# Optimization experiments

Measured on AMD Instinct MI355X. Metric: run time of the kernel, lower is better.

## Reference

```python
import jax, jax.numpy as jnp
import numpy as np

N, E = 100000, 1600000
D_IN, H, C = 128, 4, 32
NEG_SLOPE = 0.2

def setup_inputs() -> dict:
    key = jax.random.key(0)
    ks = jax.random.split(key, 6)
    x = jax.random.normal(ks[0], (N, D_IN), dtype=jnp.float32)
    edge_index = jax.random.randint(ks[1], (2, E), 0, N, dtype=jnp.int64)
    s = 1.0 / np.sqrt(D_IN)
    W_l = jax.random.normal(ks[2], (D_IN, H * C), dtype=jnp.float32) * s
    W_r = jax.random.normal(ks[3], (D_IN, H * C), dtype=jnp.float32) * s
    att = jax.random.normal(ks[4], (H, C), dtype=jnp.float32) * (1.0 / np.sqrt(C))
    bias = jax.random.normal(ks[5], (H * C,), dtype=jnp.float32) * 0.01
    return {"x": x, "edge_index": edge_index, "W_l": W_l, "W_r": W_r, "att": att, "bias": bias}

def reference(x, edge_index, W_l, W_r, att, bias):
    # GATv2: e_ij = att . LeakyReLU(W_l x_j + W_r x_i); softmax over incoming edges of i;
    # out_i = sum_j alpha_ij * (W_l x_j); heads concatenated, then bias.
    src, dst = edge_index[0], edge_index[1]
    n = x.shape[0]
    xl = (x @ W_l).reshape(n, H, C)   # source transform (lin_l)
    xr = (x @ W_r).reshape(n, H, C)   # target transform (lin_r)
    xj = xl[src]                       # [E,H,C] gathered source feats
    xi = xr[dst]                       # [E,H,C] gathered target feats
    e = jax.nn.leaky_relu(xi + xj, NEG_SLOPE)
    score = jnp.einsum('ehc,hc->eh', e, att)          # [E,H]
    # segment softmax over destination nodes
    m = jax.ops.segment_max(score, dst, num_segments=n)  # [N,H]
    ex = jnp.exp(score - m[dst])
    denom = jax.ops.segment_sum(ex, dst, num_segments=n)  # [N,H]
    alpha = ex / (denom[dst] + 1e-16)                      # [E,H]
    out = jax.ops.segment_sum(alpha[..., None] * xj, dst, num_segments=n)  # [N,H,C]
    return out.reshape(n, H * C) + bias
```

## Files before the change

### kernel.cpp

```cpp
#include <hip/hip_runtime.h>
#include <hip/hip_bf16.h>
#include <math.h>

#define N_NODES 100000
#define E_EDGES 1600000
#define D 128
#define NEG_SLOPE 0.2f

#define BSH   8
#define NBKT  391
#define BCAP  4992
#define SC_EPB 8192
#define SC_EPT 32
#define SC_BLOCKS ((E_EDGES + SC_EPB - 1) / SC_EPB)

typedef __bf16 bf16x8 __attribute__((ext_vector_type(8)));
typedef float f32x4 __attribute__((ext_vector_type(4)));
typedef float f32x2 __attribute__((ext_vector_type(2)));

__device__ __forceinline__ float bf2f(unsigned short u) {
    union { unsigned int i; float f; } x; x.i = ((unsigned int)u) << 16; return x.f;
}
__device__ __forceinline__ unsigned short f2bf(float f) {
    union { float f; unsigned int i; } x; x.f = f;
    unsigned int r = x.i + 0x7fffu + ((x.i >> 16) & 1u);
    return (unsigned short)(r >> 16);
}
__device__ __forceinline__ void unpack4p(uint2 u, f32x2* lo, f32x2* hi) {
    union { unsigned int i; float f; } a, b, c, d;
    a.i = u.x << 16; b.i = u.x & 0xffff0000u;
    c.i = u.y << 16; d.i = u.y & 0xffff0000u;
    *lo = (f32x2){a.f, b.f}; *hi = (f32x2){c.f, d.f};
}
__device__ __forceinline__ f32x2 pabs(f32x2 v) {
    union { f32x2 f; unsigned int u[2]; } x; x.f = v;
    x.u[0] &= 0x7fffffffu; x.u[1] &= 0x7fffffffu;
    return x.f;
}

__global__ void GATv2Conv_56908316672629_kernel(
    const unsigned int* ei_words, int* flags,
    const float* __restrict__ Wl, const float* __restrict__ Wr,
    unsigned short* __restrict__ wtg, int* __restrict__ bcur)
{
    __shared__ int cnt_edge;
    const int tid = threadIdx.x;
    const int bid = blockIdx.x;

    if (bid == 0) {
        for (int i = tid; i < NBKT; i += 256) bcur[i] = 0;
    }
    if (bid == 1) {
        if (tid == 0) cnt_edge = 0;
        __syncthreads();
        unsigned int w = ei_words[2 * tid + 1];
        if (w != 0u) atomicAdd(&cnt_edge, 1);
        __syncthreads();
        if (tid == 0) flags[0] = (cnt_edge == 0) ? 1 : 0;
    }

    const int gid = bid * 256 + tid;
    const int sel = gid >> 14;
    const int rem = gid & 16383;
    const int k = rem >> 7, n = rem & 127;
    const float* W = sel ? Wr : Wl;
    wtg[(size_t)sel * 16384 + n * 128 + k] = f2bf(W[k * 128 + n]);
}

__global__ __launch_bounds__(256) void gemm_f32_kernel(
    const float* __restrict__ X,
    const unsigned short* __restrict__ wtg,
    unsigned short* __restrict__ xl, unsigned short* __restrict__ xr,
    const unsigned int* __restrict__ ei, const int* __restrict__ flags,
    int* __restrict__ bcur, unsigned int* __restrict__ pairbuf)
{
    __shared__ union {
        struct {
            unsigned short Xs[128][136];
            unsigned short Cst[64][136];
        } g;
        struct { int h[NBKT]; int gbase[NBKT]; } sc;
    } sm;

    const int tid = threadIdx.x;

    if (blockIdx.x < SC_BLOCKS) {
        int* h = sm.sc.h;
        int* gbase = sm.sc.gbase;
        const int is64 = flags[0];
        const long long e0 = (long long)blockIdx.x * SC_EPB;

        unsigned int sv[SC_EPT], dv[SC_EPT];
#pragma unroll
        for (int j = 0; j < SC_EPT; ++j) {
            long long e = e0 + j * 256 + tid;
            unsigned int s = 0u, d = 0xffffffffu;
            if (e < E_EDGES) {
                if (is64) {
                    s = ((const uint2*)ei)[e].x;
                    d = ((const uint2*)ei)[E_EDGES + e].x;
                } else {
                    s = ei[e];
                    d = ei[E_EDGES + e];
                }
                if (s >= N_NODES || d >= N_NODES) d = 0xffffffffu;
            }
            sv[j] = s; dv[j] = d;
        }

        for (int i = tid; i < NBKT; i += 256) h[i] = 0;
        __syncthreads();

#pragma unroll
        for (int j = 0; j < SC_EPT; ++j)
            if (dv[j] != 0xffffffffu) atomicAdd(&h[dv[j] >> BSH], 1);
        __syncthreads();

        for (int i = tid; i < NBKT; i += 256) {
            int c = h[i];
            gbase[i] = c ? atomicAdd(&bcur[i], c) : 0;
            h[i] = 0;
        }
        __syncthreads();

#pragma unroll
        for (int j = 0; j < SC_EPT; ++j) {
            unsigned int d = dv[j];
            if (d != 0xffffffffu) {
                int b = (int)(d >> BSH);
                int r = gbase[b] + atomicAdd(&h[b], 1);
                if (r < BCAP)
                    pairbuf[(size_t)b * BCAP + r] = sv[j] | ((d & 255u) << 24);
            }
        }
        return;
    }

    const int rowbase = (blockIdx.x - SC_BLOCKS) * 128;

    for (int c = tid; c < 4096; c += 256) {
        int r = c >> 5, k4 = (c & 31) << 2;
        int grow = rowbase + r;
        float4 v = make_float4(0.f, 0.f, 0.f, 0.f);
        if (grow < N_NODES) v = ((const float4*)(X + (size_t)grow * D))[c & 31];
        union { unsigned short us[4]; uint2 u2; } pk;
        pk.us[0] = f2bf(v.x); pk.us[1] = f2bf(v.y);
        pk.us[2] = f2bf(v.z); pk.us[3] = f2bf(v.w);
        *((uint2*)&sm.g.Xs[r][k4]) = pk.u2;
    }
    __syncthreads();

    const int wave = tid >> 6, lane = tid & 63;
    const int mrow = lane & 15, quad = lane >> 4;
    const int srow = tid >> 2, sseg = tid & 3;

    for (int sel = 0; sel < 2; ++sel) {
        const bf16x8* wt = (const bf16x8*)(wtg + (size_t)sel * 16384);
        unsigned short* out = sel ? xr : xl;

        f32x4 accA[8], accB[8];
#pragma unroll
        for (int i = 0; i < 8; ++i) {
            accA[i] = (f32x4){0.f, 0.f, 0.f, 0.f};
            accB[i] = (f32x4){0.f, 0.f, 0.f, 0.f};
        }

#pragma unroll
        for (int kk = 0; kk < 4; ++kk) {
            const int k0 = kk * 32 + quad * 8;
            bf16x8 afA = *(const bf16x8*)&sm.g.Xs[wave * 16 + mrow][k0];
            bf16x8 afB = *(const bf16x8*)&sm.g.Xs[64 + wave * 16 + mrow][k0];
            const bf16x8* wk = wt + mrow * 16 + kk * 4 + quad;
#pragma unroll
            for (int n0 = 0; n0 < 8; ++n0) {
                bf16x8 bfrag = wk[n0 * 256];
                accA[n0] = __builtin_amdgcn_mfma_f32_16x16x32_bf16(afA, bfrag, accA[n0], 0, 0, 0);
                accB[n0] = __builtin_amdgcn_mfma_f32_16x16x32_bf16(afB, bfrag, accB[n0], 0, 0, 0);
            }
        }

        __syncthreads();
        const int crow = wave * 16 + quad * 4;
#pragma unroll
        for (int n0 = 0; n0 < 8; ++n0) {
            int col = n0 * 16 + mrow;
#pragma unroll
            for (int r = 0; r < 4; ++r)
                sm.g.Cst[crow + r][col] = f2bf(accA[n0][r]);
        }
        __syncthreads();
        {
            int grow = rowbase + srow;
            if (grow < N_NODES) {
                uint4* dst = (uint4*)(out + (size_t)grow * D);
#pragma unroll
                for (int j = 0; j < 4; ++j)
                    dst[sseg * 4 + j] = *(const uint4*)&sm.g.Cst[srow][sseg * 32 + j * 8];
            }
        }

        __syncthreads();
#pragma unroll
        for (int n0 = 0; n0 < 8; ++n0) {
            int col = n0 * 16 + mrow;
#pragma unroll
            for (int r = 0; r < 4; ++r)
                sm.g.Cst[crow + r][col] = f2bf(accB[n0][r]);
        }
        __syncthreads();
        {
            int grow = rowbase + 64 + srow;
            if (grow < N_NODES) {
                uint4* dst = (uint4*)(out + (size_t)grow * D);
#pragma unroll
                for (int j = 0; j < 4; ++j)
                    dst[sseg * 4 + j] = *(const uint4*)&sm.g.Cst[srow][sseg * 32 + j * 8];
            }
        }
        __syncthreads();
    }
}

__global__ __launch_bounds__(1024) void bucket_sort_kernel(
    const int* __restrict__ bcur, unsigned int* __restrict__ pairbuf,
    int* __restrict__ rowstart, int* __restrict__ rowend)
{
    __shared__ unsigned int stage[BCAP];
    __shared__ int cnt[256];
    __shared__ int wsum[4];

    const int b = blockIdx.x;
    const int tid = threadIdx.x;
    int n = bcur[b]; if (n > BCAP) n = BCAP;
    unsigned int* buf = pairbuf + (size_t)b * BCAP;

    for (int i = tid; i < n; i += 1024) stage[i] = buf[i];
    if (tid < 256) cnt[tid] = 0;
    __syncthreads();

    for (int i = tid; i < n; i += 1024) atomicAdd(&cnt[stage[i] >> 24], 1);
    __syncthreads();

    const int lane = tid & 63, wid = tid >> 6;
    int v = 0, inc = 0;
    if (tid < 256) {
        v = cnt[tid];
        inc = v;
#pragma unroll
        for (int off = 1; off < 64; off <<= 1) {
            int u = __shfl_up(inc, off);
            if (lane >= off) inc += u;
        }
        if (lane == 63) wsum[wid] = inc;
    }
    __syncthreads();
    if (tid < 256) {
        int add = 0;
#pragma unroll
        for (int w = 0; w < 3; ++w)
            if (w < wid) add += wsum[w];
        const int myend = inc + add;
        const int mystart = myend - v;
        const int node = b * 256 + tid;
        if (node < N_NODES) {
            rowstart[node] = b * BCAP + mystart;
            rowend[node]   = b * BCAP + myend;
        }
        cnt[tid] = mystart;
    }
    __syncthreads();

    for (int i = tid; i < n; i += 1024) {
        unsigned int p = stage[i];
        int pos = atomicAdd(&cnt[p >> 24], 1);
        buf[pos] = p & 0x00FFFFFFu;
    }
}

__global__ __launch_bounds__(256) void aggregate_kernel(
    const unsigned short* __restrict__ xl, const unsigned short* __restrict__ xr,
    const int* __restrict__ rowstart, const int* __restrict__ rowend,
    const int* __restrict__ ssrc,
    const float* __restrict__ att, const float* __restrict__ bias,
    float* __restrict__ out)
{
    const int t = threadIdx.x & 31;
    const int node = blockIdx.x * 8 + (threadIdx.x >> 5);
    if (node >= N_NODES) return;
    const int f0 = t * 4;

    f32x2 xr0, xr1;
    unpack4p(*(const uint2*)&xr[(size_t)node * D + f0], &xr0, &xr1);
    const float4 av = *(const float4*)&att[f0];
    f32x2 a60 = (f32x2){0.6f * av.x, 0.6f * av.y};
    f32x2 a61 = (f32x2){0.6f * av.z, 0.6f * av.w};
    f32x2 a40 = (f32x2){0.4f * av.x, 0.4f * av.y};
    f32x2 a41 = (f32x2){0.4f * av.z, 0.4f * av.w};

    const uint2* xlp = (const uint2*)xl + (f0 >> 2);

    const int p0 = rowstart[node];
    const int p1 = rowend[node];

    float l = 0.f;
    f32x2 acc0 = (f32x2){0.f, 0.f}, acc1 = (f32x2){0.f, 0.f};

#define ESCORE(u, xa0, xa1, pe)                                   \
    {                                                             \
        unpack4p(u, &xa0, &xa1);                                  \
        f32x2 v0 = xa0 + xr0, v1 = xa1 + xr1;                     \
        f32x2 pp = v0 * a60;                                      \
        pp += pabs(v0) * a40;                                     \
        pp += v1 * a61;                                           \
        pp += pabs(v1) * a41;                                     \
        pe = pp.x + pp.y;                                         \
    }

    int p = p0;
    for (; p + 4 <= p1; p += 4) {
        int s0 = ssrc[p], s1 = ssrc[p + 1], s2 = ssrc[p + 2], s3 = ssrc[p + 3];
        uint2 u0 = xlp[(size_t)s0 * 32];
        uint2 u1 = xlp[(size_t)s1 * 32];
        uint2 u2 = xlp[(size_t)s2 * 32];
        uint2 u3 = xlp[(size_t)s3 * 32];
        f32x2 xa0, xa1, xb0, xb1, xc0, xc1, xd0, xd1;
        float e0, e1, e2, e3;
        ESCORE(u0, xa0, xa1, e0);
        ESCORE(u1, xb0, xb1, e1);
        ESCORE(u2, xc0, xc1, e2);
        ESCORE(u3, xd0, xd1, e3);
#pragma unroll
        for (int off = 1; off < 8; off <<= 1) {
            e0 += __shfl_xor(e0, off);
            e1 += __shfl_xor(e1, off);
            e2 += __shfl_xor(e2, off);
            e3 += __shfl_xor(e3, off);
        }
        float w0 = __expf(e0), w1 = __expf(e1), w2 = __expf(e2), w3 = __expf(e3);
        l += (w0 + w1) + (w2 + w3);
        acc0 += w0 * xa0; acc1 += w0 * xa1;
        acc0 += w1 * xb0; acc1 += w1 * xb1;
        acc0 += w2 * xc0; acc1 += w2 * xc1;
        acc0 += w3 * xd0; acc1 += w3 * xd1;
    }
    for (; p < p1; ++p) {
        int s0 = ssrc[p];
        uint2 u0 = xlp[(size_t)s0 * 32];
        f32x2 xa0, xa1;
        float e0;
        ESCORE(u0, xa0, xa1, e0);
#pragma unroll
        for (int off = 1; off < 8; off <<= 1) e0 += __shfl_xor(e0, off);
        float w0 = __expf(e0);
        l += w0;
        acc0 += w0 * xa0; acc1 += w0 * xa1;
    }
#undef ESCORE

    const float inv = (l > 0.f) ? (1.f / l) : 0.f;
    const float4 bv = *(const float4*)&bias[f0];
    float4 o;
    o.x = fmaf(acc0.x, inv, bv.x);
    o.y = fmaf(acc0.y, inv, bv.y);
    o.z = fmaf(acc1.x, inv, bv.z);
    o.w = fmaf(acc1.y, inv, bv.w);
    *(float4*)&out[(size_t)node * D + f0] = o;
}

extern "C" void kernel_launch(void* const* d_in, const int* in_sizes, int n_in,
                              void* d_out, int out_size, void* d_ws, size_t ws_size,
                              hipStream_t stream)
{
    const float*        X    = (const float*)d_in[0];
    const unsigned int* ei   = (const unsigned int*)d_in[1];
    const float*        Wl   = (const float*)d_in[2];
    const float*        Wr   = (const float*)d_in[3];
    const float*        att  = (const float*)d_in[4];
    const float*        bias = (const float*)d_in[5];

    char* ws = (char*)d_ws;
    size_t off = 0;
    unsigned short* xl = (unsigned short*)(ws + off); off += (size_t)N_NODES * D * 2;
    unsigned short* xr = (unsigned short*)(ws + off); off += (size_t)N_NODES * D * 2;
    unsigned int* pairbuf = (unsigned int*)(ws + off); off += (size_t)NBKT * BCAP * 4;
    int* rowstart = (int*)(ws + off); off += (size_t)N_NODES * 4;
    int* rowend   = (int*)(ws + off); off += (size_t)N_NODES * 4;
    int* bcur     = (int*)(ws + off); off += (size_t)((NBKT + 255) & ~255) * 4;
    int* flags    = (int*)(ws + off); off += 256;
    unsigned short* wtg = (unsigned short*)(ws + off); off += 2 * 128 * 128 * 2;

    const int gb = (N_NODES + 127) / 128;

    GATv2Conv_56908316672629_kernel<<<128, 256, 0, stream>>>(ei, flags, Wl, Wr, wtg, bcur);

    gemm_f32_kernel<<<SC_BLOCKS + gb, 256, 0, stream>>>(
        X, wtg, xl, xr, ei, flags, bcur, pairbuf);

    bucket_sort_kernel<<<NBKT, 1024, 0, stream>>>(bcur, pairbuf, rowstart, rowend);

    aggregate_kernel<<<(N_NODES + 7) / 8, 256, 0, stream>>>(
        xl, xr, rowstart, rowend, (const int*)pairbuf, att, bias, (float*)d_out);
}
```

Before: 246.2 us.

## Fuse bucket sort and aggregation into one kernel using shared-memory CSR

Merges the per-bucket counting sort with the attention aggregation. Each 1024-thread block sorts its bucket's edges into shared memory and then aggregates its 256 destination nodes, 32 at a time over 8 passes. This removes one kernel launch, the global write and reload of the sorted source indices, and the rowstart/rowend arrays. In exchange, aggregation parallelism falls to 391 blocks with heavy shared-memory use (about 42KB), which limits occupancy and latency hiding for the gathers compared with the previous 12500 small blocks.

```diff
diff --git a/kernel.cpp b/kernel.cpp
--- a/kernel.cpp
+++ b/kernel.cpp
@@ -221,18 +221,22 @@
     }
 }
 
-__global__ __launch_bounds__(1024) void bucket_sort_kernel(
-    const int* __restrict__ bcur, unsigned int* __restrict__ pairbuf,
-    int* __restrict__ rowstart, int* __restrict__ rowend)
+__global__ __launch_bounds__(1024) void sort_agg_kernel(
+    const int* __restrict__ bcur, const unsigned int* __restrict__ pairbuf,
+    const unsigned short* __restrict__ xl, const unsigned short* __restrict__ xr,
+    const float* __restrict__ att, const float* __restrict__ bias,
+    float* __restrict__ out)
 {
     __shared__ unsigned int stage[BCAP];
+    __shared__ int sorted[BCAP];
+    __shared__ int rs[256], re[256];
     __shared__ int cnt[256];
     __shared__ int wsum[4];
 
     const int b = blockIdx.x;
     const int tid = threadIdx.x;
     int n = bcur[b]; if (n > BCAP) n = BCAP;
-    unsigned int* buf = pairbuf + (size_t)b * BCAP;
+    const unsigned int* buf = pairbuf + (size_t)b * BCAP;
 
     for (int i = tid; i < n; i += 1024) stage[i] = buf[i];
     if (tid < 256) cnt[tid] = 0;
@@ -261,11 +265,8 @@
             if (w < wid) add += wsum[w];
         const int myend = inc + add;
         const int mystart = myend - v;
-        const int node = b * 256 + tid;
-        if (node < N_NODES) {
-            rowstart[node] = b * BCAP + mystart;
-            rowend[node]   = b * BCAP + myend;
-        }
+        rs[tid] = mystart;
+        re[tid] = myend;
         cnt[tid] = mystart;
     }
     __syncthreads();
@@ -273,37 +274,20 @@
     for (int i = tid; i < n; i += 1024) {
         unsigned int p = stage[i];
         int pos = atomicAdd(&cnt[p >> 24], 1);
-        buf[pos] = p & 0x00FFFFFFu;
-    }
-}
-
-__global__ __launch_bounds__(256) void aggregate_kernel(
-    const unsigned short* __restrict__ xl, const unsigned short* __restrict__ xr,
-    const int* __restrict__ rowstart, const int* __restrict__ rowend,
-    const int* __restrict__ ssrc,
-    const float* __restrict__ att, const float* __restrict__ bias,
-    float* __restrict__ out)
-{
-    const int t = threadIdx.x & 31;
-    const int node = blockIdx.x * 8 + (threadIdx.x >> 5);
-    if (node >= N_NODES) return;
+        sorted[pos] = (int)(p & 0x00FFFFFFu);
+    }
+    __syncthreads();
+
+    const int t = tid & 31;
+    const int hw = tid >> 5;
     const int f0 = t * 4;
 
-    f32x2 xr0, xr1;
-    unpack4p(*(const uint2*)&xr[(size_t)node * D + f0], &xr0, &xr1);
     const float4 av = *(const float4*)&att[f0];
-    f32x2 a60 = (f32x2){0.6f * av.x, 0.6f * av.y};
-    f32x2 a61 = (f32x2){0.6f * av.z, 0.6f * av.w};
-    f32x2 a40 = (f32x2){0.4f * av.x, 0.4f * av.y};
-    f32x2 a41 = (f32x2){0.4f * av.z, 0.4f * av.w};
-
+    const f32x2 a60 = (f32x2){0.6f * av.x, 0.6f * av.y};
+    const f32x2 a61 = (f32x2){0.6f * av.z, 0.6f * av.w};
+    const f32x2 a40 = (f32x2){0.4f * av.x, 0.4f * av.y};
+    const f32x2 a41 = (f32x2){0.4f * av.z, 0.4f * av.w};
     const uint2* xlp = (const uint2*)xl + (f0 >> 2);
-
-    const int p0 = rowstart[node];
-    const int p1 = rowend[node];
-
-    float l = 0.f;
-    f32x2 acc0 = (f32x2){0.f, 0.f}, acc1 = (f32x2){0.f, 0.f};
 
 #define ESCORE(u, xa0, xa1, pe)                                   \
     {                                                             \
@@ -316,55 +300,70 @@
         pe = pp.x + pp.y;                                         \
     }
 
-    int p = p0;
-    for (; p + 4 <= p1; p += 4) {
-        int s0 = ssrc[p], s1 = ssrc[p + 1], s2 = ssrc[p + 2], s3 = ssrc[p + 3];
-        uint2 u0 = xlp[(size_t)s0 * 32];
-        uint2 u1 = xlp[(size_t)s1 * 32];
-        uint2 u2 = xlp[(size_t)s2 * 32];
-        uint2 u3 = xlp[(size_t)s3 * 32];
-        f32x2 xa0, xa1, xb0, xb1, xc0, xc1, xd0, xd1;
-        float e0, e1, e2, e3;
-        ESCORE(u0, xa0, xa1, e0);
-        ESCORE(u1, xb0, xb1, e1);
-        ESCORE(u2, xc0, xc1, e2);
-        ESCORE(u3, xd0, xd1, e3);
-#pragma unroll
-        for (int off = 1; off < 8; off <<= 1) {
-            e0 += __shfl_xor(e0, off);
-            e1 += __shfl_xor(e1, off);
-            e2 += __shfl_xor(e2, off);
-            e3 += __shfl_xor(e3, off);
-        }
-        float w0 = __expf(e0), w1 = __expf(e1), w2 = __expf(e2), w3 = __expf(e3);
-        l += (w0 + w1) + (w2 + w3);
-        acc0 += w0 * xa0; acc1 += w0 * xa1;
-        acc0 += w1 * xb0; acc1 += w1 * xb1;
-        acc0 += w2 * xc0; acc1 += w2 * xc1;
-        acc0 += w3 * xd0; acc1 += w3 * xd1;
-    }
-    for (; p < p1; ++p) {
-        int s0 = ssrc[p];
-        uint2 u0 = xlp[(size_t)s0 * 32];
-        f32x2 xa0, xa1;
-        float e0;
-        ESCORE(u0, xa0, xa1, e0);
-#pragma unroll
-        for (int off = 1; off < 8; off <<= 1) e0 += __shfl_xor(e0, off);
-        float w0 = __expf(e0);
-        l += w0;
-        acc0 += w0 * xa0; acc1 += w0 * xa1;
+    for (int pass = 0; pass < 8; ++pass) {
+        const int local = pass * 32 + hw;
+        const int node = b * 256 + local;
+        if (node >= N_NODES) continue;
+
+        f32x2 xr0, xr1;
+        unpack4p(*(const uint2*)&xr[(size_t)node * D + f0], &xr0, &xr1);
+
+        const int p0 = rs[local];
+        const int p1 = re[local];
+
+        float l = 0.f;
+        f32x2 acc0 = (f32x2){0.f, 0.f}, acc1 = (f32x2){0.f, 0.f};
+
+        int p = p0;
+        for (; p + 4 <= p1; p += 4) {
+            int s0 = sorted[p], s1 = sorted[p + 1], s2 = sorted[p + 2], s3 = sorted[p + 3];
+            uint2 u0 = xlp[(size_t)s0 * 32];
+            uint2 u1 = xlp[(size_t)s1 * 32];
+            uint2 u2 = xlp[(size_t)s2 * 32];
+            uint2 u3 = xlp[(size_t)s3 * 32];
+            f32x2 xa0, xa1, xb0, xb1, xc0, xc1, xd0, xd1;
+            float e0, e1, e2, e3;
+            ESCORE(u0, xa0, xa1, e0);
+            ESCORE(u1, xb0, xb1, e1);
+            ESCORE(u2, xc0, xc1, e2);
+            ESCORE(u3, xd0, xd1, e3);
+#pragma unroll
+            for (int off = 1; off < 8; off <<= 1) {
+                e0 += __shfl_xor(e0, off);
+                e1 += __shfl_xor(e1, off);
+                e2 += __shfl_xor(e2, off);
+                e3 += __shfl_xor(e3, off);
+            }
+            float w0 = __expf(e0), w1 = __expf(e1), w2 = __expf(e2), w3 = __expf(e3);
+            l += (w0 + w1) + (w2 + w3);
+            acc0 += w0 * xa0; acc1 += w0 * xa1;
+            acc0 += w1 * xb0; acc1 += w1 * xb1;
+            acc0 += w2 * xc0; acc1 += w2 * xc1;
+            acc0 += w3 * xd0; acc1 += w3 * xd1;
+        }
+        for (; p < p1; ++p) {
+            int s0 = sorted[p];
+            uint2 u0 = xlp[(size_t)s0 * 32];
+            f32x2 xa0, xa1;
+            float e0;
+            ESCORE(u0, xa0, xa1, e0);
+#pragma unroll
+            for (int off = 1; off < 8; off <<= 1) e0 += __shfl_xor(e0, off);
+            float w0 = __expf(e0);
+            l += w0;
+            acc0 += w0 * xa0; acc1 += w0 * xa1;
+        }
+
+        const float inv = (l > 0.f) ? (1.f / l) : 0.f;
+        const float4 bv = *(const float4*)&bias[f0];
+        float4 o;
+        o.x = fmaf(acc0.x, inv, bv.x);
+        o.y = fmaf(acc0.y, inv, bv.y);
+        o.z = fmaf(acc1.x, inv, bv.z);
+        o.w = fmaf(acc1.y, inv, bv.w);
+        *(float4*)&out[(size_t)node * D + f0] = o;
     }
 #undef ESCORE
-
-    const float inv = (l > 0.f) ? (1.f / l) : 0.f;
-    const float4 bv = *(const float4*)&bias[f0];
-    float4 o;
-    o.x = fmaf(acc0.x, inv, bv.x);
-    o.y = fmaf(acc0.y, inv, bv.y);
-    o.z = fmaf(acc1.x, inv, bv.z);
-    o.w = fmaf(acc1.y, inv, bv.w);
-    *(float4*)&out[(size_t)node * D + f0] = o;
 }
 
 extern "C" void kernel_launch(void* const* d_in, const int* in_sizes, int n_in,
@@ -383,8 +382,6 @@
     unsigned short* xl = (unsigned short*)(ws + off); off += (size_t)N_NODES * D * 2;
     unsigned short* xr = (unsigned short*)(ws + off); off += (size_t)N_NODES * D * 2;
     unsigned int* pairbuf = (unsigned int*)(ws + off); off += (size_t)NBKT * BCAP * 4;
-    int* rowstart = (int*)(ws + off); off += (size_t)N_NODES * 4;
-    int* rowend   = (int*)(ws + off); off += (size_t)N_NODES * 4;
     int* bcur     = (int*)(ws + off); off += (size_t)((NBKT + 255) & ~255) * 4;
     int* flags    = (int*)(ws + off); off += 256;
     unsigned short* wtg = (unsigned short*)(ws + off); off += 2 * 128 * 128 * 2;
@@ -396,8 +393,6 @@
     gemm_f32_kernel<<<SC_BLOCKS + gb, 256, 0, stream>>>(
         X, wtg, xl, xr, ei, flags, bcur, pairbuf);
 
-    bucket_sort_kernel<<<NBKT, 1024, 0, stream>>>(bcur, pairbuf, rowstart, rowend);
-
-    aggregate_kernel<<<(N_NODES + 7) / 8, 256, 0, stream>>>(
-        xl, xr, rowstart, rowend, (const int*)pairbuf, att, bias, (float*)d_out);
-}
+    sort_agg_kernel<<<NBKT, 1024, 0, stream>>>(
+        bcur, pairbuf, xl, xr, att, bias, (float*)d_out);
+}
```

After: 245.3 us. Within noise of the previous version (-0.4%).
